# Optimization experiments

Measured on AMD Instinct MI355X. Metric: run time of the kernel, lower is better.

## Reference

```python
import jax, jax.numpy as jnp
import numpy as np

N, E, IN, H, C = 50000, 400000, 128, 8, 32
NEG_SLOPE = 0.2


def setup_inputs() -> dict:
    key = jax.random.key(0)
    ks = jax.random.split(key, 8)
    s = 0.1
    return {
        "x": jax.random.normal(ks[0], (N, IN), jnp.float32),
        "edge_index": jax.random.randint(ks[1], (2, E), 0, N, dtype=jnp.int32),
        "edge_attr": jax.random.normal(ks[2], (E, 1), jnp.float32),
        "batch": jnp.zeros((N,), jnp.int32),
        "W_l": jax.random.normal(ks[3], (H * C, IN), jnp.float32) * s,
        "W_r": jax.random.normal(ks[4], (H * C, IN), jnp.float32) * s,
        "W_e": jax.random.normal(ks[5], (H * C, 1), jnp.float32) * s,
        "att": jax.random.normal(ks[6], (H, C), jnp.float32) * s,
        "bias": jnp.zeros((C,), jnp.float32),
        "W_proj": jax.random.normal(ks[7], (C, IN), jnp.float32) * s,
    }


def reference(x, edge_index, edge_attr, batch, W_l, W_r, W_e, att, bias, W_proj):
    n = x.shape[0]
    # --- add self loops (PyG default), edge_attr fill = 'mean' ---
    loop = jnp.arange(n, dtype=edge_index.dtype)
    ei = jnp.concatenate([edge_index, jnp.stack([loop, loop])], axis=1)  # [2, E+N]
    loop_attr = jnp.broadcast_to(edge_attr.mean(axis=0), (n, edge_attr.shape[1]))
    ea = jnp.concatenate([edge_attr, loop_attr], axis=0)                 # [E+N, 1]
    src, dst = ei[0], ei[1]

    # --- node transforms (GATv2: separate lin_l / lin_r) ---
    x_l = (x @ W_l.T).reshape(n, H, C)   # source-side features
    x_r = (x @ W_r.T).reshape(n, H, C)   # destination-side features
    e_feat = (ea @ W_e.T).reshape(-1, H, C)  # [E+N, H, C] edge fusion

    # --- GATv2 attention logits ---
    m = x_l[src] + x_r[dst] + e_feat                 # [E+N, H, C]
    m = jax.nn.leaky_relu(m, NEG_SLOPE)
    alpha = jnp.einsum("ehc,hc->eh", m, att)         # [E+N, H]

    # --- softmax over edges grouped by destination node ---
    amax = jax.ops.segment_max(alpha, dst, num_segments=n)  # [N, H]
    aexp = jnp.exp(alpha - amax[dst])
    denom = jax.ops.segment_sum(aexp, dst, num_segments=n)
    alpha = aexp / denom[dst]                        # [E+N, H]

    # --- weighted aggregation of source messages ---
    out = jax.ops.segment_sum(x_l[src] * alpha[:, :, None], dst, num_segments=n)  # [N, H, C]
    out = out.mean(axis=1) + bias                    # concat=False -> head mean, [N, C]

    # --- relu + projected residual ---
    x_new = jax.nn.relu(out) + x @ W_proj.T          # [N, C]
    return (x_new, alpha)
```

## Files before the change

### kernel.cpp

```cpp
#include <hip/hip_runtime.h>
#include <math.h>

#define N_NODES 50000
#define N_EDGES 400000
#define EN_TOT  450000
#define IN_DIM  128
#define H_HEADS 8
#define C_CH    32
#define HC      256
#define NEG_SLOPE 0.2f

typedef __attribute__((ext_vector_type(8))) short bf16x8;
typedef __attribute__((ext_vector_type(4))) float f32x4;

#define OFF_XLB   0
#define OFF_XRB   (OFF_XLB + N_NODES * HC / 2)
#define OFF_PROJ  (OFF_XRB + N_NODES * HC / 2)
#define OFF_AEXP  (OFF_PROJ + N_NODES * C_CH)
#define OFF_DENOM (OFF_AEXP + EN_TOT * H_HEADS)
#define OFF_XBF   (OFF_DENOM + N_NODES * H_HEADS)
#define OFF_WCAT  (OFF_XBF + N_NODES * 64)
#define OFF_PART  (OFF_WCAT + 34816)
#define OFF_MEAN  (OFF_PART + 1024)
#define OFF_CEAV  (OFF_MEAN + 1)
#define OFF_CSRC  (OFF_CEAV + EN_TOT)
#define OFF_CEID  (OFF_CSRC + EN_TOT)
#define OFF_DEG   (OFF_CEID + EN_TOT)
#define OFF_OFFS  (OFF_DEG + N_NODES)
#define OFF_CUR   (OFF_OFFS + N_NODES + 1)
#define OFF_BSUM  (OFF_CUR + N_NODES)

#define SCAN_B 196

__device__ __forceinline__ unsigned f2bf(float f) {
    unsigned u = __float_as_uint(f);
    u += 0x7fffu + ((u >> 16) & 1u);
    return u >> 16;
}
__device__ __forceinline__ float bflo(unsigned u) { return __uint_as_float(u << 16); }
__device__ __forceinline__ float bfhi(unsigned u) { return __uint_as_float(u & 0xffff0000u); }

#define XCHUNKS 800000
#define WCHUNKS 8704
__global__ __launch_bounds__(256) void convert_kernel(
    const float* __restrict__ x,
    const float* __restrict__ Wl, const float* __restrict__ Wr, const float* __restrict__ Wproj,
    unsigned short* __restrict__ xbf, unsigned short* __restrict__ wcat)
{
    int t = blockIdx.x * 256 + threadIdx.x;
    const float* src; uint4* dst;
    if (t < XCHUNKS) {
        src = x + (size_t)t * 8;
        dst = (uint4*)xbf + t;
    } else if (t < XCHUNKS + WCHUNKS) {
        int c = t - XCHUNKS;
        int j = (c * 8) >> 7, k = (c * 8) & 127;
        src = (j < 256 ? Wl + (size_t)j * 128 : (j < 512 ? Wr + (size_t)(j - 256) * 128
                                                         : Wproj + (size_t)(j - 512) * 128)) + k;
        dst = (uint4*)wcat + c;
    } else return;
    float4 a = ((const float4*)src)[0];
    float4 b = ((const float4*)src)[1];
    uint4 o;
    o.x = f2bf(a.x) | (f2bf(a.y) << 16);
    o.y = f2bf(a.z) | (f2bf(a.w) << 16);
    o.z = f2bf(b.x) | (f2bf(b.y) << 16);
    o.w = f2bf(b.z) | (f2bf(b.w) << 16);
    *dst = o;
}

__global__ __launch_bounds__(256) void hist_mean_kernel(
    const int* __restrict__ ei, const float* __restrict__ ea,
    int* __restrict__ deg, float* __restrict__ part)
{
    __shared__ float sd[256];
    int t = threadIdx.x;
    int g = blockIdx.x * 256 + t;
    float s = 0.f;
    for (int i = g; i < N_EDGES; i += 1024 * 256) s += ea[i];
    for (int i = g; i < EN_TOT; i += 1024 * 256) {
        int d = (i < N_EDGES) ? ei[N_EDGES + i] : (i - N_EDGES);
        atomicAdd(&deg[d], 1);
    }
    sd[t] = s; __syncthreads();
    for (int w = 128; w > 0; w >>= 1) { if (t < w) sd[t] += sd[t + w]; __syncthreads(); }
    if (t == 0) part[blockIdx.x] = sd[0];
}

__global__ void mean_final_kernel(const float* __restrict__ part, float* __restrict__ mean_out) {
    __shared__ float sd[256];
    int t = threadIdx.x;
    float s = part[t] + part[t + 256] + part[t + 512] + part[t + 768];
    sd[t] = s; __syncthreads();
    for (int w = 128; w > 0; w >>= 1) { if (t < w) sd[t] += sd[t + w]; __syncthreads(); }
    if (t == 0) mean_out[0] = sd[0] / (float)N_EDGES;
}

__global__ __launch_bounds__(256) void scan_part_kernel(const int* __restrict__ deg,
                                                        int* __restrict__ bsum) {
    __shared__ int sd[256];
    int t = threadIdx.x;
    int i = blockIdx.x * 256 + t;
    int v = (i < N_NODES) ? deg[i] : 0;
    sd[t] = v; __syncthreads();
    for (int w = 128; w > 0; w >>= 1) { if (t < w) sd[t] += sd[t + w]; __syncthreads(); }
    if (t == 0) bsum[blockIdx.x] = sd[0];
}

__global__ __launch_bounds__(256) void scan_mid_kernel(int* __restrict__ bsum) {
    __shared__ int sd[256];
    int t = threadIdx.x;
    int v = (t < SCAN_B) ? bsum[t] : 0;
    sd[t] = v; __syncthreads();
    #pragma unroll
    for (int ofs = 1; ofs < 256; ofs <<= 1) {
        int u = (t >= ofs) ? sd[t - ofs] : 0;
        __syncthreads();
        sd[t] += u;
        __syncthreads();
    }
    if (t < SCAN_B) bsum[t] = sd[t] - v;
}

__global__ __launch_bounds__(256) void scan_final_kernel(
    const int* __restrict__ deg, const int* __restrict__ bsum,
    int* __restrict__ offs, int* __restrict__ cur) {
    __shared__ int sd[256];
    int t = threadIdx.x;
    int i = blockIdx.x * 256 + t;
    int v = (i < N_NODES) ? deg[i] : 0;
    sd[t] = v; __syncthreads();
    #pragma unroll
    for (int ofs = 1; ofs < 256; ofs <<= 1) {
        int u = (t >= ofs) ? sd[t - ofs] : 0;
        __syncthreads();
        sd[t] += u;
        __syncthreads();
    }
    int excl = bsum[blockIdx.x] + sd[t] - v;
    if (i < N_NODES) { offs[i] = excl; cur[i] = excl; }
    if (i == N_NODES - 1) offs[N_NODES] = excl + v;
}

__global__ __launch_bounds__(256) void scatter_kernel(
    const int* __restrict__ ei, const float* __restrict__ edge_attr,
    const float* __restrict__ mean_attr, int* __restrict__ cur,
    int* __restrict__ csr_src, int* __restrict__ csr_eid, float* __restrict__ csr_eav)
{
    int e = blockIdx.x * 256 + threadIdx.x;
    if (e >= EN_TOT) return;
    int s, d; float eav;
    if (e < N_EDGES) { s = ei[e]; d = ei[N_EDGES + e]; eav = edge_attr[e]; }
    else { s = e - N_EDGES; d = s; eav = mean_attr[0]; }
    int pos = atomicAdd(&cur[d], 1);
    csr_src[pos] = s;
    csr_eid[pos] = e;
    csr_eav[pos] = eav;
}

#define GM 128
#define GN 64

__global__ __launch_bounds__(256) void gemm_mfma_kernel(
    const unsigned short* __restrict__ xbf, const unsigned short* __restrict__ wcat,
    unsigned short* __restrict__ xlb, unsigned short* __restrict__ xrb,
    float* __restrict__ proj)
{
    __shared__ unsigned short As[GM * 128];
    __shared__ unsigned short Bs[GN * 128];
    const int t = threadIdx.x;
    const int m0 = blockIdx.x * GM;
    const int n0 = blockIdx.y * GN;

    #pragma unroll
    for (int cc = 0; cc < 8; ++cc) {
        int c = t + cc * 256;
        int r = c >> 4;
        int k0 = (c & 15) * 8;
        int row = m0 + r;
        uint4 v = make_uint4(0, 0, 0, 0);
        if (row < N_NODES) v = *((const uint4*)(xbf + (size_t)row * 128 + k0));
        int byte = (r * 256 + k0 * 2) ^ ((r & 7) << 4);
        *((uint4*)((char*)As + byte)) = v;
    }
    #pragma unroll
    for (int cc = 0; cc < 4; ++cc) {
        int c = t + cc * 256;
        int r = c >> 4;
        int k0 = (c & 15) * 8;
        int j = n0 + r;
        uint4 v = make_uint4(0, 0, 0, 0);
        if (j < 544) v = *((const uint4*)(wcat + (size_t)j * 128 + k0));
        int byte = (r * 256 + k0 * 2) ^ ((r & 7) << 4);
        *((uint4*)((char*)Bs + byte)) = v;
    }
    __syncthreads();

    const int wid = t >> 6, lane = t & 63;
    const int wr = wid >> 1, wc = wid & 1;
    const int lrow = lane & 15;
    const int kgrp = (lane >> 4) * 8;

    f32x4 acc[4][2] = {};
    #pragma unroll
    for (int kk = 0; kk < 4; ++kk) {
        bf16x8 a[4], b[2];
        #pragma unroll
        for (int fm = 0; fm < 4; ++fm) {
            int r = wr * 64 + fm * 16 + lrow;
            int byte = (r * 256 + (kk * 32 + kgrp) * 2) ^ ((r & 7) << 4);
            a[fm] = *((const bf16x8*)((const char*)As + byte));
        }
        #pragma unroll
        for (int fn = 0; fn < 2; ++fn) {
            int r = wc * 32 + fn * 16 + lrow;
            int byte = (r * 256 + (kk * 32 + kgrp) * 2) ^ ((r & 7) << 4);
            b[fn] = *((const bf16x8*)((const char*)Bs + byte));
        }
        #pragma unroll
        for (int fm = 0; fm < 4; ++fm)
            #pragma unroll
            for (int fn = 0; fn < 2; ++fn)
                acc[fm][fn] = __builtin_amdgcn_mfma_f32_16x16x32_bf16(a[fm], b[fn], acc[fm][fn], 0, 0, 0);
    }

    const int crow0 = (lane >> 4) * 4;
    const int ccol = lane & 15;
    #pragma unroll
    for (int fm = 0; fm < 4; ++fm) {
        #pragma unroll
        for (int fn = 0; fn < 2; ++fn) {
            #pragma unroll
            for (int r = 0; r < 4; ++r) {
                int row = m0 + wr * 64 + fm * 16 + crow0 + r;
                int col = n0 + wc * 32 + fn * 16 + ccol;
                if (row >= N_NODES) continue;
                float v = acc[fm][fn][r];
                if (col < 256)      xlb[(size_t)row * HC + col] = (unsigned short)f2bf(v);
                else if (col < 512) xrb[(size_t)row * HC + (col - 256)] = (unsigned short)f2bf(v);
                else if (col < 544) proj[(size_t)row * C_CH + (col - 512)] = v;
            }
        }
    }
}

__global__ __launch_bounds__(256) void node_agg_kernel(
    const int* __restrict__ offs, const int* __restrict__ csr_src,
    const int* __restrict__ csr_eid, const float* __restrict__ csr_eav,
    const float* __restrict__ We, const float* __restrict__ att,
    const unsigned short* __restrict__ xlb, const unsigned short* __restrict__ xrb,
    const float* __restrict__ proj, const float* __restrict__ bias,
    float* __restrict__ aexp_out, float* __restrict__ denom, float* __restrict__ xnew)
{
    const int lane = threadIdx.x & 63;
    const int d = blockIdx.x * 4 + (threadIdx.x >> 6);
    if (d >= N_NODES) return;

    const float4 we = ((const float4*)We)[lane];
    const float4 at = ((const float4*)att)[lane];
    const uint2 vru = ((const uint2*)(xrb + (size_t)d * HC))[lane];
    const float vr0 = bflo(vru.x), vr1 = bfhi(vru.x), vr2 = bflo(vru.y), vr3 = bfhi(vru.y);
    const int h = lane >> 3;

    float4 acc = make_float4(0.f, 0.f, 0.f, 0.f);
    float den = 0.f;

    int i = offs[d];
    const int end = offs[d + 1];

    int e0 = 0; float ea0 = 0.f; uint2 vl0 = make_uint2(0, 0);
    if (i < end) {
        int s0 = csr_src[i]; e0 = csr_eid[i]; ea0 = csr_eav[i];
        vl0 = ((const uint2*)(xlb + (size_t)s0 * HC))[lane];
    }
    while (i < end) {
        const int j = i + 1;
        int e1 = 0; float ea1 = 0.f; uint2 vl1 = make_uint2(0, 0);
        if (j < end) {
            int s1 = csr_src[j]; e1 = csr_eid[j]; ea1 = csr_eav[j];
            vl1 = ((const uint2*)(xlb + (size_t)s1 * HC))[lane];
        }

        const float x0 = bflo(vl0.x), x1 = bfhi(vl0.x), x2 = bflo(vl0.y), x3 = bfhi(vl0.y);
        float m0 = x0 + vr0 + ea0 * we.x;
        float m1 = x1 + vr1 + ea0 * we.y;
        float m2 = x2 + vr2 + ea0 * we.z;
        float m3 = x3 + vr3 + ea0 * we.w;
        m0 = (m0 > 0.f) ? m0 : NEG_SLOPE * m0;
        m1 = (m1 > 0.f) ? m1 : NEG_SLOPE * m1;
        m2 = (m2 > 0.f) ? m2 : NEG_SLOPE * m2;
        m3 = (m3 > 0.f) ? m3 : NEG_SLOPE * m3;
        float tt = m0 * at.x + m1 * at.y + m2 * at.z + m3 * at.w;
        tt += __shfl_xor(tt, 1);
        tt += __shfl_xor(tt, 2);
        tt += __shfl_xor(tt, 4);
        const float aex = __expf(tt);

        if ((lane & 7) == 0) aexp_out[(size_t)e0 * H_HEADS + h] = aex;
        acc.x += aex * x0; acc.y += aex * x1;
        acc.z += aex * x2; acc.w += aex * x3;
        den += aex;

        e0 = e1; ea0 = ea1; vl0 = vl1; i = j;
    }

    if ((lane & 7) == 0) denom[(size_t)d * H_HEADS + h] = den;

    const float inv = 1.f / den;
    acc.x *= inv; acc.y *= inv; acc.z *= inv; acc.w *= inv;
    #pragma unroll
    for (int mask = 8; mask <= 32; mask <<= 1) {
        acc.x += __shfl_xor(acc.x, mask);
        acc.y += __shfl_xor(acc.y, mask);
        acc.z += __shfl_xor(acc.z, mask);
        acc.w += __shfl_xor(acc.w, mask);
    }
    if (lane < 8) {
        const float4 bi = ((const float4*)bias)[lane];
        const float4 pr = ((const float4*)(proj + (size_t)d * C_CH))[lane];
        float4 r;
        r.x = fmaxf(acc.x * 0.125f + bi.x, 0.f) + pr.x;
        r.y = fmaxf(acc.y * 0.125f + bi.y, 0.f) + pr.y;
        r.z = fmaxf(acc.z * 0.125f + bi.z, 0.f) + pr.z;
        r.w = fmaxf(acc.w * 0.125f + bi.w, 0.f) + pr.w;
        ((float4*)(xnew + (size_t)d * C_CH))[lane] = r;
    }
}

__global__ __launch_bounds__(256) void alpha_kernel(
    const int* __restrict__ ei, const float* __restrict__ aexp,
    const float* __restrict__ denom, float* __restrict__ alpha_out)
{
    int idx = blockIdx.x * 256 + threadIdx.x;
    if (idx >= EN_TOT * H_HEADS) return;
    int e = idx >> 3, h = idx & 7;
    int d = (e < N_EDGES) ? ei[N_EDGES + e] : (e - N_EDGES);
    alpha_out[idx] = aexp[idx] / denom[(size_t)d * H_HEADS + h];
}

extern "C" void kernel_launch(void* const* d_in, const int* in_sizes, int n_in,
                              void* d_out, int out_size, void* d_ws, size_t ws_size,
                              hipStream_t stream) {
    const float* x         = (const float*)d_in[0];
    const int*   ei        = (const int*)d_in[1];
    const float* edge_attr = (const float*)d_in[2];
    const float* Wl        = (const float*)d_in[4];
    const float* Wr        = (const float*)d_in[5];
    const float* We        = (const float*)d_in[6];
    const float* att       = (const float*)d_in[7];
    const float* bias      = (const float*)d_in[8];
    const float* Wproj     = (const float*)d_in[9];

    float* ws    = (float*)d_ws;
    unsigned short* xlb  = (unsigned short*)(ws + OFF_XLB);
    unsigned short* xrb  = (unsigned short*)(ws + OFF_XRB);
    float* proj  = ws + OFF_PROJ;
    float* aexp  = ws + OFF_AEXP;
    float* denom = ws + OFF_DENOM;
    unsigned short* xbf  = (unsigned short*)(ws + OFF_XBF);
    unsigned short* wcat = (unsigned short*)(ws + OFF_WCAT);
    float* part  = ws + OFF_PART;
    float* meanp = ws + OFF_MEAN;
    float* ceav  = ws + OFF_CEAV;
    int*   csrc  = (int*)(ws + OFF_CSRC);
    int*   ceid  = (int*)(ws + OFF_CEID);
    int*   deg   = (int*)(ws + OFF_DEG);
    int*   offs  = (int*)(ws + OFF_OFFS);
    int*   cur   = (int*)(ws + OFF_CUR);
    int*   bsum  = (int*)(ws + OFF_BSUM);

    float* out_xnew  = (float*)d_out;
    float* out_alpha = (float*)d_out + (size_t)N_NODES * C_CH;

    hipMemsetAsync(deg, 0, N_NODES * sizeof(int), stream);

    convert_kernel<<<(XCHUNKS + WCHUNKS + 255) / 256, 256, 0, stream>>>(x, Wl, Wr, Wproj, xbf, wcat);

    hist_mean_kernel<<<1024, 256, 0, stream>>>(ei, edge_attr, deg, part);
    mean_final_kernel<<<1, 256, 0, stream>>>(part, meanp);

    scan_part_kernel<<<SCAN_B, 256, 0, stream>>>(deg, bsum);
    scan_mid_kernel<<<1, 256, 0, stream>>>(bsum);
    scan_final_kernel<<<SCAN_B, 256, 0, stream>>>(deg, bsum, offs, cur);

    scatter_kernel<<<(EN_TOT + 255) / 256, 256, 0, stream>>>(ei, edge_attr, meanp, cur,
                                                             csrc, ceid, ceav);

    dim3 ggrid((N_NODES + GM - 1) / GM, (544 + GN - 1) / GN);
    gemm_mfma_kernel<<<ggrid, 256, 0, stream>>>(xbf, wcat, xlb, xrb, proj);

    node_agg_kernel<<<(N_NODES + 3) / 4, 256, 0, stream>>>(offs, csrc, ceid, ceav,
                                                           We, att, xlb, xrb, proj, bias,
                                                           aexp, denom, out_xnew);

    alpha_kernel<<<(EN_TOT * H_HEADS + 255) / 256, 256, 0, stream>>>(ei, aexp, denom, out_alpha);
}
```

Measured before the change: 204.0 us.

## Fuse x bf16 conversion into GEMM, pack CSR, fuse alpha normalization into aggregation

Removes the separate x-to-bf16 conversion pass by converting fp32 x on the fly while loading GEMM tiles. CSR arrays are packed into one int4 record per edge so each edge needs a single load. The aggregation kernel now processes two edges per wavefront iteration with 8 channels per lane, then normalizes alpha in-kernel, which drops the denom buffer and the separate alpha kernel. The trade-off is that the GEMM re-reads and reconverts fp32 x for each of its 9 column-block tiles, and aexp is read back right after being written.

```diff
diff --git a/kernel.cpp b/kernel.cpp
--- a/kernel.cpp
+++ b/kernel.cpp
@@ -14,18 +14,15 @@
 typedef __attribute__((ext_vector_type(4))) float f32x4;
 
 #define OFF_XLB   0
-#define OFF_XRB   (OFF_XLB + N_NODES * HC / 2)
-#define OFF_PROJ  (OFF_XRB + N_NODES * HC / 2)
+#define OFF_XRB   (OFF_XLB + N_NODES * 128)
+#define OFF_PROJ  (OFF_XRB + N_NODES * 128)
 #define OFF_AEXP  (OFF_PROJ + N_NODES * C_CH)
-#define OFF_DENOM (OFF_AEXP + EN_TOT * H_HEADS)
-#define OFF_XBF   (OFF_DENOM + N_NODES * H_HEADS)
-#define OFF_WCAT  (OFF_XBF + N_NODES * 64)
+#define OFF_WCAT  (OFF_AEXP + EN_TOT * H_HEADS)
 #define OFF_PART  (OFF_WCAT + 34816)
 #define OFF_MEAN  (OFF_PART + 1024)
-#define OFF_CEAV  (OFF_MEAN + 1)
-#define OFF_CSRC  (OFF_CEAV + EN_TOT)
-#define OFF_CEID  (OFF_CSRC + EN_TOT)
-#define OFF_DEG   (OFF_CEID + EN_TOT)
+#define OFF_PAD   (OFF_MEAN + 1)
+#define OFF_CSR4  (OFF_PAD + 3)
+#define OFF_DEG   (OFF_CSR4 + EN_TOT * 4)
 #define OFF_OFFS  (OFF_DEG + N_NODES)
 #define OFF_CUR   (OFF_OFFS + N_NODES + 1)
 #define OFF_BSUM  (OFF_CUR + N_NODES)
@@ -40,25 +37,17 @@
 __device__ __forceinline__ float bflo(unsigned u) { return __uint_as_float(u << 16); }
 __device__ __forceinline__ float bfhi(unsigned u) { return __uint_as_float(u & 0xffff0000u); }
 
-#define XCHUNKS 800000
 #define WCHUNKS 8704
-__global__ __launch_bounds__(256) void convert_kernel(
-    const float* __restrict__ x,
+__global__ __launch_bounds__(256) void convert_w_kernel(
     const float* __restrict__ Wl, const float* __restrict__ Wr, const float* __restrict__ Wproj,
-    unsigned short* __restrict__ xbf, unsigned short* __restrict__ wcat)
+    unsigned short* __restrict__ wcat)
 {
-    int t = blockIdx.x * 256 + threadIdx.x;
-    const float* src; uint4* dst;
-    if (t < XCHUNKS) {
-        src = x + (size_t)t * 8;
-        dst = (uint4*)xbf + t;
-    } else if (t < XCHUNKS + WCHUNKS) {
-        int c = t - XCHUNKS;
-        int j = (c * 8) >> 7, k = (c * 8) & 127;
-        src = (j < 256 ? Wl + (size_t)j * 128 : (j < 512 ? Wr + (size_t)(j - 256) * 128
-                                                         : Wproj + (size_t)(j - 512) * 128)) + k;
-        dst = (uint4*)wcat + c;
-    } else return;
+    int c = blockIdx.x * 256 + threadIdx.x;
+    if (c >= WCHUNKS) return;
+    int j = (c * 8) >> 7, k = (c * 8) & 127;
+    const float* src = (j < 256 ? Wl + (size_t)j * 128
+                                : (j < 512 ? Wr + (size_t)(j - 256) * 128
+                                           : Wproj + (size_t)(j - 512) * 128)) + k;
     float4 a = ((const float4*)src)[0];
     float4 b = ((const float4*)src)[1];
     uint4 o;
@@ -66,7 +55,7 @@
     o.y = f2bf(a.z) | (f2bf(a.w) << 16);
     o.z = f2bf(b.x) | (f2bf(b.y) << 16);
     o.w = f2bf(b.z) | (f2bf(b.w) << 16);
-    *dst = o;
+    ((uint4*)wcat)[c] = o;
 }
 
 __global__ __launch_bounds__(256) void hist_mean_kernel(
@@ -145,7 +134,7 @@
 __global__ __launch_bounds__(256) void scatter_kernel(
     const int* __restrict__ ei, const float* __restrict__ edge_attr,
     const float* __restrict__ mean_attr, int* __restrict__ cur,
-    int* __restrict__ csr_src, int* __restrict__ csr_eid, float* __restrict__ csr_eav)
+    int4* __restrict__ csr4)
 {
     int e = blockIdx.x * 256 + threadIdx.x;
     if (e >= EN_TOT) return;
@@ -153,16 +142,14 @@
     if (e < N_EDGES) { s = ei[e]; d = ei[N_EDGES + e]; eav = edge_attr[e]; }
     else { s = e - N_EDGES; d = s; eav = mean_attr[0]; }
     int pos = atomicAdd(&cur[d], 1);
-    csr_src[pos] = s;
-    csr_eid[pos] = e;
-    csr_eav[pos] = eav;
+    csr4[pos] = make_int4(s, e, __float_as_int(eav), 0);
 }
 
 #define GM 128
 #define GN 64
 
 __global__ __launch_bounds__(256) void gemm_mfma_kernel(
-    const unsigned short* __restrict__ xbf, const unsigned short* __restrict__ wcat,
+    const float* __restrict__ x, const unsigned short* __restrict__ wcat,
     unsigned short* __restrict__ xlb, unsigned short* __restrict__ xrb,
     float* __restrict__ proj)
 {
@@ -178,10 +165,18 @@
         int r = c >> 4;
         int k0 = (c & 15) * 8;
         int row = m0 + r;
-        uint4 v = make_uint4(0, 0, 0, 0);
-        if (row < N_NODES) v = *((const uint4*)(xbf + (size_t)row * 128 + k0));
+        uint4 o = make_uint4(0, 0, 0, 0);
+        if (row < N_NODES) {
+            const float* p = x + (size_t)row * IN_DIM + k0;
+            float4 a = ((const float4*)p)[0];
+            float4 b = ((const float4*)p)[1];
+            o.x = f2bf(a.x) | (f2bf(a.y) << 16);
+            o.y = f2bf(a.z) | (f2bf(a.w) << 16);
+            o.z = f2bf(b.x) | (f2bf(b.y) << 16);
+            o.w = f2bf(b.z) | (f2bf(b.w) << 16);
+        }
         int byte = (r * 256 + k0 * 2) ^ ((r & 7) << 4);
-        *((uint4*)((char*)As + byte)) = v;
+        *((uint4*)((char*)As + byte)) = o;
     }
     #pragma unroll
     for (int cc = 0; cc < 4; ++cc) {
@@ -245,97 +240,117 @@
 }
 
 __global__ __launch_bounds__(256) void node_agg_kernel(
-    const int* __restrict__ offs, const int* __restrict__ csr_src,
-    const int* __restrict__ csr_eid, const float* __restrict__ csr_eav,
+    const int* __restrict__ offs, const int4* __restrict__ csr4,
     const float* __restrict__ We, const float* __restrict__ att,
     const unsigned short* __restrict__ xlb, const unsigned short* __restrict__ xrb,
     const float* __restrict__ proj, const float* __restrict__ bias,
-    float* __restrict__ aexp_out, float* __restrict__ denom, float* __restrict__ xnew)
+    float* __restrict__ aexp_out, float* __restrict__ alpha_out, float* __restrict__ xnew)
 {
-    const int lane = threadIdx.x & 63;
+    const int l = threadIdx.x & 63;
     const int d = blockIdx.x * 4 + (threadIdx.x >> 6);
     if (d >= N_NODES) return;
-
-    const float4 we = ((const float4*)We)[lane];
-    const float4 at = ((const float4*)att)[lane];
-    const uint2 vru = ((const uint2*)(xrb + (size_t)d * HC))[lane];
-    const float vr0 = bflo(vru.x), vr1 = bfhi(vru.x), vr2 = bflo(vru.y), vr3 = bfhi(vru.y);
-    const int h = lane >> 3;
-
-    float4 acc = make_float4(0.f, 0.f, 0.f, 0.f);
+    const int half = l >> 5;
+    const int sl = l & 31;
+
+    const float4 we0 = ((const float4*)We)[sl * 2];
+    const float4 we1 = ((const float4*)We)[sl * 2 + 1];
+    const float4 at0 = ((const float4*)att)[sl * 2];
+    const float4 at1 = ((const float4*)att)[sl * 2 + 1];
+    const float wev[8] = {we0.x, we0.y, we0.z, we0.w, we1.x, we1.y, we1.z, we1.w};
+    const float atv[8] = {at0.x, at0.y, at0.z, at0.w, at1.x, at1.y, at1.z, at1.w};
+
+    const uint4 vru = ((const uint4*)(xrb + (size_t)d * HC))[sl];
+    float vr[8];
+    vr[0] = bflo(vru.x); vr[1] = bfhi(vru.x); vr[2] = bflo(vru.y); vr[3] = bfhi(vru.y);
+    vr[4] = bflo(vru.z); vr[5] = bfhi(vru.z); vr[6] = bflo(vru.w); vr[7] = bfhi(vru.w);
+
+    const int beg = offs[d];
+    const int end = offs[d + 1];
+
+    float acc[8] = {0.f, 0.f, 0.f, 0.f, 0.f, 0.f, 0.f, 0.f};
     float den = 0.f;
 
-    int i = offs[d];
-    const int end = offs[d + 1];
-
-    int e0 = 0; float ea0 = 0.f; uint2 vl0 = make_uint2(0, 0);
-    if (i < end) {
-        int s0 = csr_src[i]; e0 = csr_eid[i]; ea0 = csr_eav[i];
-        vl0 = ((const uint2*)(xlb + (size_t)s0 * HC))[lane];
+    int i = beg;
+    int4 c0 = make_int4(0, 0, 0, 0);
+    uint4 vl0 = make_uint4(0, 0, 0, 0);
+    if (i + half < end) {
+        c0 = csr4[i + half];
+        vl0 = ((const uint4*)(xlb + (size_t)c0.x * HC))[sl];
     }
     while (i < end) {
-        const int j = i + 1;
-        int e1 = 0; float ea1 = 0.f; uint2 vl1 = make_uint2(0, 0);
-        if (j < end) {
-            int s1 = csr_src[j]; e1 = csr_eid[j]; ea1 = csr_eav[j];
-            vl1 = ((const uint2*)(xlb + (size_t)s1 * HC))[lane];
-        }
-
-        const float x0 = bflo(vl0.x), x1 = bfhi(vl0.x), x2 = bflo(vl0.y), x3 = bfhi(vl0.y);
-        float m0 = x0 + vr0 + ea0 * we.x;
-        float m1 = x1 + vr1 + ea0 * we.y;
-        float m2 = x2 + vr2 + ea0 * we.z;
-        float m3 = x3 + vr3 + ea0 * we.w;
-        m0 = (m0 > 0.f) ? m0 : NEG_SLOPE * m0;
-        m1 = (m1 > 0.f) ? m1 : NEG_SLOPE * m1;
-        m2 = (m2 > 0.f) ? m2 : NEG_SLOPE * m2;
-        m3 = (m3 > 0.f) ? m3 : NEG_SLOPE * m3;
-        float tt = m0 * at.x + m1 * at.y + m2 * at.z + m3 * at.w;
+        const int ni = i + 2;
+        int4 c1 = make_int4(0, 0, 0, 0);
+        uint4 vl1 = make_uint4(0, 0, 0, 0);
+        if (ni + half < end) {
+            c1 = csr4[ni + half];
+            vl1 = ((const uint4*)(xlb + (size_t)c1.x * HC))[sl];
+        }
+
+        const float ea = __int_as_float(c0.z);
+        float xv[8];
+        xv[0] = bflo(vl0.x); xv[1] = bfhi(vl0.x); xv[2] = bflo(vl0.y); xv[3] = bfhi(vl0.y);
+        xv[4] = bflo(vl0.z); xv[5] = bfhi(vl0.z); xv[6] = bflo(vl0.w); xv[7] = bfhi(vl0.w);
+
+        float tt = 0.f;
+        #pragma unroll
+        for (int j = 0; j < 8; ++j) {
+            float m = xv[j] + vr[j] + ea * wev[j];
+            m = fmaxf(m, NEG_SLOPE * m);
+            tt += m * atv[j];
+        }
         tt += __shfl_xor(tt, 1);
         tt += __shfl_xor(tt, 2);
-        tt += __shfl_xor(tt, 4);
-        const float aex = __expf(tt);
-
-        if ((lane & 7) == 0) aexp_out[(size_t)e0 * H_HEADS + h] = aex;
-        acc.x += aex * x0; acc.y += aex * x1;
-        acc.z += aex * x2; acc.w += aex * x3;
+        float aex = __expf(tt);
+        const bool valid = (i + half) < end;
+        aex = valid ? aex : 0.f;
+        if (valid && (sl & 3) == 0)
+            aexp_out[(size_t)c0.y * H_HEADS + (sl >> 2)] = aex;
+        #pragma unroll
+        for (int j = 0; j < 8; ++j) acc[j] += aex * xv[j];
         den += aex;
 
-        e0 = e1; ea0 = ea1; vl0 = vl1; i = j;
-    }
-
-    if ((lane & 7) == 0) denom[(size_t)d * H_HEADS + h] = den;
+        c0 = c1; vl0 = vl1; i = ni;
+    }
+
+    den += __shfl_xor(den, 32);
+    #pragma unroll
+    for (int j = 0; j < 8; ++j) acc[j] += __shfl_xor(acc[j], 32);
+
+    const float den_h = __shfl(den, ((l & 7) << 2));
+    const float rden = 1.f / den_h;
+    for (int b = beg; b < end; b += 8) {
+        const int idx = b + (l >> 3);
+        if (idx < end) {
+            const int e = csr4[idx].y;
+            const float ax = aexp_out[(size_t)e * H_HEADS + (l & 7)];
+            alpha_out[(size_t)e * H_HEADS + (l & 7)] = ax * rden;
+        }
+    }
 
     const float inv = 1.f / den;
-    acc.x *= inv; acc.y *= inv; acc.z *= inv; acc.w *= inv;
-    #pragma unroll
-    for (int mask = 8; mask <= 32; mask <<= 1) {
-        acc.x += __shfl_xor(acc.x, mask);
-        acc.y += __shfl_xor(acc.y, mask);
-        acc.z += __shfl_xor(acc.z, mask);
-        acc.w += __shfl_xor(acc.w, mask);
-    }
-    if (lane < 8) {
-        const float4 bi = ((const float4*)bias)[lane];
-        const float4 pr = ((const float4*)(proj + (size_t)d * C_CH))[lane];
-        float4 r;
-        r.x = fmaxf(acc.x * 0.125f + bi.x, 0.f) + pr.x;
-        r.y = fmaxf(acc.y * 0.125f + bi.y, 0.f) + pr.y;
-        r.z = fmaxf(acc.z * 0.125f + bi.z, 0.f) + pr.z;
-        r.w = fmaxf(acc.w * 0.125f + bi.w, 0.f) + pr.w;
-        ((float4*)(xnew + (size_t)d * C_CH))[lane] = r;
-    }
-}
-
-__global__ __launch_bounds__(256) void alpha_kernel(
-    const int* __restrict__ ei, const float* __restrict__ aexp,
-    const float* __restrict__ denom, float* __restrict__ alpha_out)
-{
-    int idx = blockIdx.x * 256 + threadIdx.x;
-    if (idx >= EN_TOT * H_HEADS) return;
-    int e = idx >> 3, h = idx & 7;
-    int d = (e < N_EDGES) ? ei[N_EDGES + e] : (e - N_EDGES);
-    alpha_out[idx] = aexp[idx] / denom[(size_t)d * H_HEADS + h];
+    #pragma unroll
+    for (int j = 0; j < 8; ++j) acc[j] *= inv;
+    #pragma unroll
+    for (int mask = 4; mask <= 16; mask <<= 1)
+        #pragma unroll
+        for (int j = 0; j < 8; ++j) acc[j] += __shfl_xor(acc[j], mask);
+    if (half == 0 && sl < 4) {
+        const float4 bi0 = ((const float4*)bias)[sl * 2];
+        const float4 bi1 = ((const float4*)bias)[sl * 2 + 1];
+        const float4 pr0 = ((const float4*)(proj + (size_t)d * C_CH))[sl * 2];
+        const float4 pr1 = ((const float4*)(proj + (size_t)d * C_CH))[sl * 2 + 1];
+        float4 r0, r1;
+        r0.x = fmaxf(acc[0] * 0.125f + bi0.x, 0.f) + pr0.x;
+        r0.y = fmaxf(acc[1] * 0.125f + bi0.y, 0.f) + pr0.y;
+        r0.z = fmaxf(acc[2] * 0.125f + bi0.z, 0.f) + pr0.z;
+        r0.w = fmaxf(acc[3] * 0.125f + bi0.w, 0.f) + pr0.w;
+        r1.x = fmaxf(acc[4] * 0.125f + bi1.x, 0.f) + pr1.x;
+        r1.y = fmaxf(acc[5] * 0.125f + bi1.y, 0.f) + pr1.y;
+        r1.z = fmaxf(acc[6] * 0.125f + bi1.z, 0.f) + pr1.z;
+        r1.w = fmaxf(acc[7] * 0.125f + bi1.w, 0.f) + pr1.w;
+        ((float4*)(xnew + (size_t)d * C_CH))[sl * 2] = r0;
+        ((float4*)(xnew + (size_t)d * C_CH))[sl * 2 + 1] = r1;
+    }
 }
 
 extern "C" void kernel_launch(void* const* d_in, const int* in_sizes, int n_in,
@@ -356,14 +371,10 @@
     unsigned short* xrb  = (unsigned short*)(ws + OFF_XRB);
     float* proj  = ws + OFF_PROJ;
     float* aexp  = ws + OFF_AEXP;
-    float* denom = ws + OFF_DENOM;
-    unsigned short* xbf  = (unsigned short*)(ws + OFF_XBF);
     unsigned short* wcat = (unsigned short*)(ws + OFF_WCAT);
     float* part  = ws + OFF_PART;
     float* meanp = ws + OFF_MEAN;
-    float* ceav  = ws + OFF_CEAV;
-    int*   csrc  = (int*)(ws + OFF_CSRC);
-    int*   ceid  = (int*)(ws + OFF_CEID);
+    int4*  csr4  = (int4*)(ws + OFF_CSR4);
     int*   deg   = (int*)(ws + OFF_DEG);
     int*   offs  = (int*)(ws + OFF_OFFS);
     int*   cur   = (int*)(ws + OFF_CUR);
@@ -374,7 +385,7 @@
 
     hipMemsetAsync(deg, 0, N_NODES * sizeof(int), stream);
 
-    convert_kernel<<<(XCHUNKS + WCHUNKS + 255) / 256, 256, 0, stream>>>(x, Wl, Wr, Wproj, xbf, wcat);
+    convert_w_kernel<<<(WCHUNKS + 255) / 256, 256, 0, stream>>>(Wl, Wr, Wproj, wcat);
 
     hist_mean_kernel<<<1024, 256, 0, stream>>>(ei, edge_attr, deg, part);
     mean_final_kernel<<<1, 256, 0, stream>>>(part, meanp);
@@ -383,15 +394,11 @@
     scan_mid_kernel<<<1, 256, 0, stream>>>(bsum);
     scan_final_kernel<<<SCAN_B, 256, 0, stream>>>(deg, bsum, offs, cur);
 
-    scatter_kernel<<<(EN_TOT + 255) / 256, 256, 0, stream>>>(ei, edge_attr, meanp, cur,
-                                                             csrc, ceid, ceav);
+    scatter_kernel<<<(EN_TOT + 255) / 256, 256, 0, stream>>>(ei, edge_attr, meanp, cur, csr4);
 
     dim3 ggrid((N_NODES + GM - 1) / GM, (544 + GN - 1) / GN);
-    gemm_mfma_kernel<<<ggrid, 256, 0, stream>>>(xbf, wcat, xlb, xrb, proj);
-
-    node_agg_kernel<<<(N_NODES + 3) / 4, 256, 0, stream>>>(offs, csrc, ceid, ceav,
-                                                           We, att, xlb, xrb, proj, bias,
-                                                           aexp, denom, out_xnew);
-
-    alpha_kernel<<<(EN_TOT * H_HEADS + 255) / 256, 256, 0, stream>>>(ei, aexp, denom, out_alpha);
-}
+    gemm_mfma_kernel<<<ggrid, 256, 0, stream>>>(x, wcat, xlb, xrb, proj);
+
+    node_agg_kernel<<<(N_NODES + 3) / 4, 256, 0, stream>>>(offs, csr4, We, att, xlb, xrb,
+                                                           proj, bias, aexp, out_alpha, out_xnew);
+}
```

After: 186.4 us. -8.6%, faster.
